# Kernel optimization log

Measured on AMD Instinct MI355X. Metric: run time of the kernel, lower is better.

The kernel has to match this reference:

```python
import jax, jax.numpy as jnp
import numpy as np

N = 50000      # total nodes
E = 800000     # total edges
G = 1000       # graphs in batch
H = 128        # in_channels == hidden_channels
L = 3          # num GCN layers
C = 6          # num classes
EPS = 1e-5     # BatchNorm eps


def setup_inputs() -> dict:
    key = jax.random.key(0)
    ks = jax.random.split(key, 8)
    x = jax.random.normal(ks[0], (N, H), jnp.float32)
    edge_index = jax.random.randint(ks[1], (2, E), 0, N)
    batch = jnp.sort(jax.random.randint(ks[2], (N,), 0, G))
    conv_w = jax.random.normal(ks[3], (L, H, H), jnp.float32) * 0.05
    conv_b = jnp.zeros((L, H), jnp.float32)
    bn_g = jnp.ones((L, H), jnp.float32)
    bn_b = jnp.zeros((L, H), jnp.float32)
    mlp_w1 = jax.random.normal(ks[4], (H, H), jnp.float32) * 0.05
    mlp_b1 = jnp.zeros((H,), jnp.float32)
    mlp_w2 = jax.random.normal(ks[5], (H, C), jnp.float32) * 0.05
    mlp_b2 = jnp.zeros((C,), jnp.float32)
    return {"x": x, "edge_index": edge_index, "batch": batch,
            "conv_w": conv_w, "conv_b": conv_b, "bn_g": bn_g, "bn_b": bn_b,
            "mlp_w1": mlp_w1, "mlp_b1": mlp_b1, "mlp_w2": mlp_w2, "mlp_b2": mlp_b2}


def reference(x, edge_index, batch, conv_w, conv_b, bn_g, bn_b, mlp_w1, mlp_b1, mlp_w2, mlp_b2):
    src, dst = edge_index[0], edge_index[1]
    # GCN symmetric norm with self-loops: deg over A+I
    deg = jax.ops.segment_sum(jnp.ones((E,), x.dtype), dst, num_segments=N) + 1.0
    dis = jax.lax.rsqrt(deg)                      # deg^{-1/2}, [N]
    edge_norm = (dis[src] * dis[dst])[:, None]    # [E,1]
    self_norm = (dis * dis)[:, None]              # [N,1] self-loop weight 1/deg

    for l in range(L):
        h = x @ conv_w[l]                                             # [N,H]
        agg = jax.ops.segment_sum(h[src] * edge_norm, dst, num_segments=N)
        h = agg + h * self_norm + conv_b[l]
        # BatchNorm (training-mode batch statistics, biased var)
        mu = jnp.mean(h, axis=0)
        var = jnp.var(h, axis=0)
        hn = (h - mu) * jax.lax.rsqrt(var + EPS)
        x = jax.nn.relu(hn * bn_g[l] + bn_b[l])   # dropout = identity (eval)

    # global mean pool per graph
    sums = jax.ops.segment_sum(x, batch, num_segments=G)              # [G,H]
    cnt = jax.ops.segment_sum(jnp.ones((N,), x.dtype), batch, num_segments=G)
    pooled = sums / jnp.maximum(cnt, 1.0)[:, None]

    h = jax.nn.relu(pooled @ mlp_w1 + mlp_b1)
    return h @ mlp_w2 + mlp_b2                                         # [G,C]
```

## Files before the change

### kernel.cpp

```cpp
#include <hip/hip_runtime.h>

#define Nn 50000
#define Ee 800000
#define Gg 1000
#define Hh 128
#define Cc 6
#define EPSf 1e-5f
#define SB 1024
#define NSB ((Nn + SB - 1) / SB)
#define NBH 64
#define EPB (Ee / NBH)
#define NW (Nn / 2)
#define HWH (NW / 2)

typedef unsigned short u16;
typedef unsigned int u32;
typedef __attribute__((ext_vector_type(8))) short bf16x8;
typedef __attribute__((ext_vector_type(4))) float f32x4;
typedef __attribute__((ext_vector_type(4))) unsigned int u32x4;

static __device__ inline u16 f2bf(float f) {
    u32 u = __float_as_uint(f);
    u32 r = (u + 0x7fffu + ((u >> 16) & 1u)) >> 16;
    return (u16)r;
}
static __device__ inline float bf_lo(u32 v) { return __uint_as_float(v << 16); }
static __device__ inline float bf_hi(u32 v) { return __uint_as_float(v & 0xffff0000u); }
static __device__ inline u32 pack2(float a, float b) {
    return ((u32)f2bf(b) << 16) | (u32)f2bf(a);
}

__global__ __launch_bounds__(256) void k_pre(const float* __restrict__ W3,
                                             u16* __restrict__ WT3,
                                             float* __restrict__ stats3) {
    int t = blockIdx.x * blockDim.x + threadIdx.x;
    if (t < 3 * 2 * Hh) stats3[t] = 0.0f;

    __shared__ u16 tbuf[Hh * 136];
    int l = blockIdx.x;
    const float* W = W3 + l * Hh * Hh;
    u16* WT = WT3 + l * Hh * Hh;
    int tid = threadIdx.x;
#pragma unroll
    for (int i = 0; i < 16; i++) {
        int v = tid + 256 * i;
        int r = v >> 5, c4 = v & 31;
        float4 d = ((const float4*)W)[v];
        u16* p = tbuf + r * 136 + c4 * 4;
        p[0] = f2bf(d.x); p[1] = f2bf(d.y); p[2] = f2bf(d.z); p[3] = f2bf(d.w);
    }
    __syncthreads();
#pragma unroll
    for (int i = 0; i < 64; i++) {
        int o = tid + 256 * i;
        int n = o >> 7, k = o & 127;
        WT[o] = tbuf[k * 136 + n];
    }
}

__global__ __launch_bounds__(1024) void k_hist(const int* __restrict__ ei_dst,
                                               u16* __restrict__ rankL,
                                               u32* __restrict__ partials) {
    __shared__ u32 h[HWH];
    int b = blockIdx.x, t = threadIdx.x;
    int e0 = b * EPB;
    u32* P = partials + b * NW;
#pragma unroll 1
    for (int half = 0; half < 2; half++) {
        int wlo = half * HWH;
        for (int i = t; i < HWH; i += 1024) h[i] = 0u;
        __syncthreads();
        for (int i = t; i < EPB; i += 1024) {
            int d = ei_dst[e0 + i];
            int w = d >> 1;
            if (w >= wlo && w < wlo + HWH) {
                u32 old = atomicAdd(&h[w - wlo], (d & 1) ? 65536u : 1u);
                rankL[e0 + i] = (u16)((d & 1) ? (old >> 16) : (old & 0xffffu));
            }
        }
        __syncthreads();
        for (int i = t; i < HWH; i += 1024) P[wlo + i] = h[i];
        __syncthreads();
    }
}

__global__ __launch_bounds__(256) void k_merge(const u32* __restrict__ partials,
                                               u32* __restrict__ base_off,
                                               int* __restrict__ indeg) {
    int w = blockIdx.x * 256 + threadIdx.x;
    if (w >= NW) return;
    u32 run = 0;
#pragma unroll 8
    for (int b = 0; b < NBH; b++) {
        u32 v = partials[b * NW + w];
        base_off[b * NW + w] = run;
        run += v;
    }
    ((int2*)indeg)[w] = make_int2((int)(run & 0xffffu), (int)(run >> 16));
}

__global__ __launch_bounds__(256) void k_scan1(const int* __restrict__ indeg,
                                               int* __restrict__ rs,
                                               int* __restrict__ bsum,
                                               float* __restrict__ dis,
                                               const int* __restrict__ batch,
                                               int* __restrict__ gstart) {
    __shared__ int ts[256];
    int b = blockIdx.x;
    int t = threadIdx.x;
    int base = b * SB + t * 4;
    int v[4] = {0, 0, 0, 0};
#pragma unroll
    for (int j = 0; j < 4; j++) {
        int i = base + j;
        if (i < Nn) { v[j] = indeg[i]; dis[i] = rsqrtf((float)v[j] + 1.0f); }
    }
    int g = b * 256 + t;
    if (g <= Gg) {
        int lo = 0, hi = Nn;
        while (lo < hi) {
            int mid = (lo + hi) >> 1;
            if (batch[mid] < g) lo = mid + 1; else hi = mid;
        }
        gstart[g] = lo;
    }
    int tsum = v[0] + v[1] + v[2] + v[3];
    ts[t] = tsum;
    __syncthreads();
    for (int off = 1; off < 256; off <<= 1) {
        int x = (t >= off) ? ts[t - off] : 0;
        __syncthreads();
        ts[t] += x;
        __syncthreads();
    }
    int run = (t == 0) ? 0 : ts[t - 1];
    if (t == 255) bsum[b] = ts[255];
#pragma unroll
    for (int j = 0; j < 4; j++) {
        int i = base + j;
        if (i < Nn) { rs[i] = run; run += v[j]; }
    }
}

__global__ __launch_bounds__(256) void k_scan2(int* __restrict__ rs,
                                               const int* __restrict__ bsum) {
    __shared__ int lboff[NSB];
    int t = threadIdx.x;
    if (t < 64) {
        int orig = (t < NSB) ? bsum[t] : 0;
        int v = orig;
#pragma unroll
        for (int off = 1; off < 64; off <<= 1) {
            int u = __shfl_up(v, off, 64);
            if (t >= off) v += u;
        }
        if (t < NSB) lboff[t] = v - orig;
    }
    __syncthreads();
    int i = blockIdx.x * blockDim.x + t;
    if (i < Nn) rs[i] += lboff[i >> 10];
    if (blockIdx.x == 0 && t == 0) rs[Nn] = Ee;
}

__global__ void k_fill(const int* __restrict__ ei, const int* __restrict__ rs,
                       const u16* __restrict__ rankL,
                       const u32* __restrict__ base_off,
                       const float* __restrict__ dis, u32* __restrict__ recs) {
    int e = blockIdx.x * blockDim.x + threadIdx.x;
    if (e >= Ee) return;
    int s = ei[e];
    int d = ei[Ee + e];
    int blk = e / EPB;
    u32 bo = base_off[blk * NW + (d >> 1)];
    int rank = (int)rankL[e] + (int)((d & 1) ? (bo >> 16) : (bo & 0xffffu));
    int slot = rs[d] + rank;
    float w = dis[s] * dis[d];
    recs[slot] = ((u32)f2bf(w) << 16) | (u32)s;
}

__global__ __launch_bounds__(256) void k_gemm(const u16* __restrict__ Xin,
                                              const float* __restrict__ Xf,
                                              const u16* __restrict__ WT,
                                              u16* __restrict__ Yh,
                                              const float* __restrict__ stats,
                                              const float* __restrict__ gam,
                                              const float* __restrict__ bet,
                                              int mode) {
    __shared__ u16 wt[Hh * 136];
    __shared__ float s_scale[Hh], s_shift[Hh];
    int tid = threadIdx.x;

    if (mode == 1 && tid < Hh) {
        float mu = stats[tid] * (1.0f / Nn);
        float var = stats[Hh + tid] * (1.0f / Nn) - mu * mu;
        float sc = rsqrtf(var + EPSf) * gam[tid];
        s_scale[tid] = sc;
        s_shift[tid] = bet[tid] - mu * sc;
    }
#pragma unroll
    for (int i = 0; i < 8; i++) {
        int v = tid + 256 * i;
        int n = v >> 4, k8 = v & 15;
        uint4 d = ((const uint4*)WT)[v];
        *((uint4*)(wt + n * 136 + k8 * 8)) = d;
    }
    __syncthreads();

    int wv = tid >> 6, lane = tid & 63;
    int m = lane & 15, q = lane >> 4;
    int row0 = blockIdx.x * 64 + wv * 16;
    int lrow = row0 + m;
    if (lrow >= Nn) lrow = Nn - 1;
    const u16* xrow = Xin + lrow * Hh + q * 8;
    const float* xfrow = Xf + lrow * Hh + q * 8;

    f32x4 acc[8] = {};
#pragma unroll
    for (int k0 = 0; k0 < Hh; k0 += 32) {
        bf16x8 a;
        if (mode == 1) {
            int cb = k0 + q * 8;
            uint4 p = *(const uint4*)(xrow + k0);
            float4 sc0 = *(const float4*)(s_scale + cb);
            float4 sc1 = *(const float4*)(s_scale + cb + 4);
            float4 sh0 = *(const float4*)(s_shift + cb);
            float4 sh1 = *(const float4*)(s_shift + cb + 4);
            float f0 = fmaxf(bf_lo(p.x) * sc0.x + sh0.x, 0.0f);
            float f1 = fmaxf(bf_hi(p.x) * sc0.y + sh0.y, 0.0f);
            float f2 = fmaxf(bf_lo(p.y) * sc0.z + sh0.z, 0.0f);
            float f3 = fmaxf(bf_hi(p.y) * sc0.w + sh0.w, 0.0f);
            float f4 = fmaxf(bf_lo(p.z) * sc1.x + sh1.x, 0.0f);
            float f5 = fmaxf(bf_hi(p.z) * sc1.y + sh1.y, 0.0f);
            float f6 = fmaxf(bf_lo(p.w) * sc1.z + sh1.z, 0.0f);
            float f7 = fmaxf(bf_hi(p.w) * sc1.w + sh1.w, 0.0f);
            union { bf16x8 v; u32 u[4]; } cv;
            cv.u[0] = pack2(f0, f1);
            cv.u[1] = pack2(f2, f3);
            cv.u[2] = pack2(f4, f5);
            cv.u[3] = pack2(f6, f7);
            a = cv.v;
        } else {
            float4 u0 = *(const float4*)(xfrow + k0);
            float4 u1 = *(const float4*)(xfrow + k0 + 4);
            union { bf16x8 v; u32 u[4]; } cv;
            cv.u[0] = pack2(u0.x, u0.y);
            cv.u[1] = pack2(u0.z, u0.w);
            cv.u[2] = pack2(u1.x, u1.y);
            cv.u[3] = pack2(u1.z, u1.w);
            a = cv.v;
        }
#pragma unroll
        for (int t = 0; t < 8; t++) {
            bf16x8 b = *(const bf16x8*)(wt + (t * 16 + m) * 136 + k0 + q * 8);
            acc[t] = __builtin_amdgcn_mfma_f32_16x16x32_bf16(a, b, acc[t], 0, 0, 0);
        }
    }

    int orow0 = row0 + q * 4;
#pragma unroll
    for (int t = 0; t < 8; t++) {
#pragma unroll
        for (int r = 0; r < 4; r++) {
            int rr = orow0 + r;
            if (rr < Nn) Yh[rr * Hh + t * 16 + m] = f2bf(acc[t][r]);
        }
    }
}

__global__ __launch_bounds__(256) void k_gather(const u16* __restrict__ Yh,
                                                const float* __restrict__ dis,
                                                const float* __restrict__ bias,
                                                const int* __restrict__ rs,
                                                const u32* __restrict__ recs,
                                                u16* __restrict__ Ah) {
    int node = blockIdx.x * 4 + (threadIdx.x >> 6);
    if (node >= Nn) return;
    int lane = threadIdx.x & 63;
    int lg = lane >> 4;
    int lc = lane & 15;

    const uint4* rows4 = (const uint4*)Yh;

    float acc[8] = {0.f, 0.f, 0.f, 0.f, 0.f, 0.f, 0.f, 0.f};

    int beg = rs[node];
    int end = rs[node + 1];

    for (int base = beg; base < end; base += 64) {
        int me = base + lane;
        u32 myrec = recs[me < end ? me : end - 1];
        int cnt = end - base;
        if (cnt > 64) cnt = 64;
        for (int i0 = 0; i0 < cnt; i0 += 16) {
            u32 rr[4]; float ww[4]; uint4 vv[4];
#pragma unroll
            for (int j = 0; j < 4; j++) {
                int si = i0 + j * 4 + lg;
                int sc = si < cnt ? si : cnt - 1;
                u32 rec = __shfl(myrec, sc, 64);
                rr[j] = rec & 0xffffu;
                ww[j] = (si < cnt) ? __uint_as_float(rec & 0xffff0000u) : 0.0f;
            }
#pragma unroll
            for (int j = 0; j < 4; j++) vv[j] = rows4[rr[j] * 16 + lc];
#pragma unroll
            for (int j = 0; j < 4; j++) {
                acc[0] += bf_lo(vv[j].x) * ww[j];
                acc[1] += bf_hi(vv[j].x) * ww[j];
                acc[2] += bf_lo(vv[j].y) * ww[j];
                acc[3] += bf_hi(vv[j].y) * ww[j];
                acc[4] += bf_lo(vv[j].z) * ww[j];
                acc[5] += bf_hi(vv[j].z) * ww[j];
                acc[6] += bf_lo(vv[j].w) * ww[j];
                acc[7] += bf_hi(vv[j].w) * ww[j];
            }
        }
    }
#pragma unroll
    for (int k = 0; k < 8; k++) {
        acc[k] += __shfl_xor(acc[k], 16, 64);
        acc[k] += __shfl_xor(acc[k], 32, 64);
    }
    if (lg == 0) {
        float sn = dis[node];
        sn = sn * sn;
        uint4 hv = rows4[node * 16 + lc];
        const float4* bq = (const float4*)bias;
        float4 b0 = bq[lc * 2];
        float4 b1 = bq[lc * 2 + 1];
        acc[0] = acc[0] + bf_lo(hv.x) * sn + b0.x;
        acc[1] = acc[1] + bf_hi(hv.x) * sn + b0.y;
        acc[2] = acc[2] + bf_lo(hv.y) * sn + b0.z;
        acc[3] = acc[3] + bf_hi(hv.y) * sn + b0.w;
        acc[4] = acc[4] + bf_lo(hv.z) * sn + b1.x;
        acc[5] = acc[5] + bf_hi(hv.z) * sn + b1.y;
        acc[6] = acc[6] + bf_lo(hv.w) * sn + b1.z;
        acc[7] = acc[7] + bf_hi(hv.w) * sn + b1.w;
        u32x4 o;
        o.x = pack2(acc[0], acc[1]);
        o.y = pack2(acc[2], acc[3]);
        o.z = pack2(acc[4], acc[5]);
        o.w = pack2(acc[6], acc[7]);
        __builtin_nontemporal_store(o, (u32x4*)Ah + node * 16 + lc);
    }
}

__global__ __launch_bounds__(256) void k_stats(const u16* __restrict__ Ah,
                                               float* __restrict__ stats) {
    __shared__ float sh[4][256];
    int t = threadIdx.x;
    int jc = t & 63, ro = t >> 6;
    const u32* col = (const u32*)Ah + jc;
    float sx = 0.f, sy = 0.f, qx = 0.f, qy = 0.f;
    for (int r = blockIdx.x * 16 + ro * 4; r < Nn; r += 4096) {
        u32 v[4];
#pragma unroll
        for (int k = 0; k < 4; k++) {
            int rr = r + k;
            v[k] = (rr < Nn) ? col[rr * 64] : 0u;
        }
#pragma unroll
        for (int k = 0; k < 4; k++) {
            float a = bf_lo(v[k]), b = bf_hi(v[k]);
            sx += a; sy += b; qx += a * a; qy += b * b;
        }
    }
    sh[0][t] = sx; sh[1][t] = sy; sh[2][t] = qx; sh[3][t] = qy;
    __syncthreads();
    if (t < 64) {
        sx = sh[0][t] + sh[0][t + 64] + sh[0][t + 128] + sh[0][t + 192];
        sy = sh[1][t] + sh[1][t + 64] + sh[1][t + 128] + sh[1][t + 192];
        qx = sh[2][t] + sh[2][t + 64] + sh[2][t + 128] + sh[2][t + 192];
        qy = sh[3][t] + sh[3][t + 64] + sh[3][t + 128] + sh[3][t + 192];
        atomicAdd(&stats[2 * t], sx);
        atomicAdd(&stats[2 * t + 1], sy);
        atomicAdd(&stats[Hh + 2 * t], qx);
        atomicAdd(&stats[Hh + 2 * t + 1], qy);
    }
}

__global__ __launch_bounds__(128) void k_poolmlp(const u16* __restrict__ Ah,
                                                 const float* __restrict__ stats,
                                                 const float* __restrict__ gam,
                                                 const float* __restrict__ bet,
                                                 const int* __restrict__ gstart,
                                                 const float* __restrict__ W1,
                                                 const float* __restrict__ b1,
                                                 const float* __restrict__ W2,
                                                 const float* __restrict__ b2,
                                                 float* __restrict__ out) {
    int g = blockIdx.x;
    int c = threadIdx.x;
    __shared__ float p[Hh];
    __shared__ float hid[Hh];
    float mu = stats[c] * (1.0f / Nn);
    float var = stats[Hh + c] * (1.0f / Nn) - mu * mu;
    float sc = rsqrtf(var + EPSf) * gam[c];
    float sf = bet[c] - mu * sc;
    int s = gstart[g], e = gstart[g + 1];
    float sum0 = 0.0f, sum1 = 0.0f;
    int r = s;
    for (; r + 1 < e; r += 2) {
        float v0 = __uint_as_float((u32)Ah[r * Hh + c] << 16);
        float v1 = __uint_as_float((u32)Ah[(r + 1) * Hh + c] << 16);
        sum0 += fmaxf(v0 * sc + sf, 0.0f);
        sum1 += fmaxf(v1 * sc + sf, 0.0f);
    }
    if (r < e) {
        float v = __uint_as_float((u32)Ah[r * Hh + c] << 16);
        sum0 += fmaxf(v * sc + sf, 0.0f);
    }
    int n = e - s;
    p[c] = (sum0 + sum1) / (float)(n > 1 ? n : 1);
    __syncthreads();
    float acc = b1[c];
    for (int k = 0; k < Hh; k++) acc += p[k] * W1[k * Hh + c];
    hid[c] = fmaxf(acc, 0.0f);
    __syncthreads();
    if (c < Cc) {
        float acc2 = b2[c];
        for (int k = 0; k < Hh; k++) acc2 += hid[k] * W2[k * Cc + c];
        out[g * Cc + c] = acc2;
    }
}

extern "C" void kernel_launch(void* const* d_in, const int* in_sizes, int n_in,
                              void* d_out, int out_size, void* d_ws, size_t ws_size,
                              hipStream_t stream) {
    const float* x      = (const float*)d_in[0];
    const int*   ei     = (const int*)d_in[1];
    const int*   batch  = (const int*)d_in[2];
    const float* conv_w = (const float*)d_in[3];
    const float* conv_b = (const float*)d_in[4];
    const float* bn_g   = (const float*)d_in[5];
    const float* bn_b   = (const float*)d_in[6];
    const float* w1     = (const float*)d_in[7];
    const float* b1     = (const float*)d_in[8];
    const float* w2     = (const float*)d_in[9];
    const float* b2     = (const float*)d_in[10];
    float* out = (float*)d_out;

    u16*   Yh      = (u16*)d_ws;
    u16*   Ah      = Yh + Nn * Hh;
    u16*   WT      = Ah + Nn * Hh;
    float* dis     = (float*)(WT + 3 * Hh * Hh);
    float* stats3  = dis + Nn;
    int*   indeg   = (int*)(stats3 + 3 * 2 * Hh);
    int*   rs      = indeg + Nn;
    int*   gstart  = rs + Nn + 1;
    int*   bsum    = gstart + Gg + 1;
    u32*   recs    = (u32*)(bsum + NSB);
    u16*   rankL   = (u16*)(recs + Ee);
    u32*   partials = (u32*)(rankL + Ee);
    u32*   base_off = partials + NBH * NW;

    k_pre<<<3, 256, 0, stream>>>(conv_w, WT, stats3);
    k_gemm<<<(Nn + 63) / 64, 256, 0, stream>>>(nullptr, x, WT, Yh,
                                               nullptr, nullptr, nullptr, 2);
    k_hist<<<NBH, 1024, 0, stream>>>(ei + Ee, rankL, partials);
    k_merge<<<(NW + 255) / 256, 256, 0, stream>>>(partials, base_off, indeg);
    k_scan1<<<NSB, 256, 0, stream>>>(indeg, rs, bsum, dis, batch, gstart);
    k_scan2<<<(Nn + 255) / 256, 256, 0, stream>>>(rs, bsum);
    k_fill<<<(Ee + 255) / 256, 256, 0, stream>>>(ei, rs, rankL, base_off, dis, recs);

    for (int l = 0; l < 3; l++) {
        k_gather<<<(Nn + 3) / 4, 256, 0, stream>>>(Yh, dis, conv_b + l * Hh, rs,
                                                   recs, Ah);
        k_stats<<<256, 256, 0, stream>>>(Ah, stats3 + l * 2 * Hh);
        if (l < 2) {
            k_gemm<<<(Nn + 63) / 64, 256, 0, stream>>>(Ah, nullptr,
                                                       WT + (l + 1) * Hh * Hh, Yh,
                                                       stats3 + l * 2 * Hh,
                                                       bn_g + l * Hh, bn_b + l * Hh, 1);
        }
    }

    k_poolmlp<<<Gg, 128, 0, stream>>>(Ah, stats3 + 2 * 2 * Hh, bn_g + 2 * Hh,
                                      bn_b + 2 * Hh, gstart, w1, b1, w2, b2, out);
}
```

Before: 331.0 us.

## Fuse per-layer gather/stats/GEMM into one cooperative persistent kernel; merge histogram merge into scan

The three GCN layers' gather, BatchNorm statistics and next-layer GEMM launches are replaced by one cooperative persistent kernel with 768 blocks. Grid-wide syncs separate the phases and blocks loop over nodes and tiles. Separately, the k_merge kernel is folded into k_scan1, so each scan thread computes the per-node degree prefix directly from the histogram partials. This removes about eight kernel launches and their gaps, at the cost of grid.sync overhead and a fixed grid size that may underfill or imbalance the gather phase.

```diff
diff --git a/kernel.cpp b/kernel.cpp
--- a/kernel.cpp
+++ b/kernel.cpp
@@ -1,4 +1,7 @@
 #include <hip/hip_runtime.h>
+#include <hip/hip_cooperative_groups.h>
+
+namespace cg = cooperative_groups;
 
 #define Nn 50000
 #define Ee 800000
@@ -12,6 +15,7 @@
 #define EPB (Ee / NBH)
 #define NW (Nn / 2)
 #define HWH (NW / 2)
+#define LGRID 768
 
 typedef unsigned short u16;
 typedef unsigned int u32;
@@ -84,22 +88,8 @@
     }
 }
 
-__global__ __launch_bounds__(256) void k_merge(const u32* __restrict__ partials,
+__global__ __launch_bounds__(256) void k_scan1(const u32* __restrict__ partials,
                                                u32* __restrict__ base_off,
-                                               int* __restrict__ indeg) {
-    int w = blockIdx.x * 256 + threadIdx.x;
-    if (w >= NW) return;
-    u32 run = 0;
-#pragma unroll 8
-    for (int b = 0; b < NBH; b++) {
-        u32 v = partials[b * NW + w];
-        base_off[b * NW + w] = run;
-        run += v;
-    }
-    ((int2*)indeg)[w] = make_int2((int)(run & 0xffffu), (int)(run >> 16));
-}
-
-__global__ __launch_bounds__(256) void k_scan1(const int* __restrict__ indeg,
                                                int* __restrict__ rs,
                                                int* __restrict__ bsum,
                                                float* __restrict__ dis,
@@ -110,10 +100,23 @@
     int t = threadIdx.x;
     int base = b * SB + t * 4;
     int v[4] = {0, 0, 0, 0};
-#pragma unroll
-    for (int j = 0; j < 4; j++) {
-        int i = base + j;
-        if (i < Nn) { v[j] = indeg[i]; dis[i] = rsqrtf((float)v[j] + 1.0f); }
+    if (base < Nn) {
+        int w0 = base >> 1;
+        u32 run0 = 0, run1 = 0;
+#pragma unroll 8
+        for (int b2 = 0; b2 < NBH; b2++) {
+            u32 p0 = partials[b2 * NW + w0];
+            u32 p1 = partials[b2 * NW + w0 + 1];
+            base_off[b2 * NW + w0] = run0;
+            base_off[b2 * NW + w0 + 1] = run1;
+            run0 += p0; run1 += p1;
+        }
+        v[0] = (int)(run0 & 0xffffu); v[1] = (int)(run0 >> 16);
+        v[2] = (int)(run1 & 0xffffu); v[3] = (int)(run1 >> 16);
+        dis[base]     = rsqrtf((float)v[0] + 1.0f);
+        dis[base + 1] = rsqrtf((float)v[1] + 1.0f);
+        dis[base + 2] = rsqrtf((float)v[2] + 1.0f);
+        dis[base + 3] = rsqrtf((float)v[3] + 1.0f);
     }
     int g = b * 256 + t;
     if (g <= Gg) {
@@ -178,114 +181,17 @@
     recs[slot] = ((u32)f2bf(w) << 16) | (u32)s;
 }
 
-__global__ __launch_bounds__(256) void k_gemm(const u16* __restrict__ Xin,
-                                              const float* __restrict__ Xf,
-                                              const u16* __restrict__ WT,
-                                              u16* __restrict__ Yh,
-                                              const float* __restrict__ stats,
-                                              const float* __restrict__ gam,
-                                              const float* __restrict__ bet,
-                                              int mode) {
-    __shared__ u16 wt[Hh * 136];
-    __shared__ float s_scale[Hh], s_shift[Hh];
-    int tid = threadIdx.x;
-
-    if (mode == 1 && tid < Hh) {
-        float mu = stats[tid] * (1.0f / Nn);
-        float var = stats[Hh + tid] * (1.0f / Nn) - mu * mu;
-        float sc = rsqrtf(var + EPSf) * gam[tid];
-        s_scale[tid] = sc;
-        s_shift[tid] = bet[tid] - mu * sc;
-    }
-#pragma unroll
-    for (int i = 0; i < 8; i++) {
-        int v = tid + 256 * i;
-        int n = v >> 4, k8 = v & 15;
-        uint4 d = ((const uint4*)WT)[v];
-        *((uint4*)(wt + n * 136 + k8 * 8)) = d;
-    }
-    __syncthreads();
-
-    int wv = tid >> 6, lane = tid & 63;
-    int m = lane & 15, q = lane >> 4;
-    int row0 = blockIdx.x * 64 + wv * 16;
-    int lrow = row0 + m;
-    if (lrow >= Nn) lrow = Nn - 1;
-    const u16* xrow = Xin + lrow * Hh + q * 8;
-    const float* xfrow = Xf + lrow * Hh + q * 8;
-
-    f32x4 acc[8] = {};
-#pragma unroll
-    for (int k0 = 0; k0 < Hh; k0 += 32) {
-        bf16x8 a;
-        if (mode == 1) {
-            int cb = k0 + q * 8;
-            uint4 p = *(const uint4*)(xrow + k0);
-            float4 sc0 = *(const float4*)(s_scale + cb);
-            float4 sc1 = *(const float4*)(s_scale + cb + 4);
-            float4 sh0 = *(const float4*)(s_shift + cb);
-            float4 sh1 = *(const float4*)(s_shift + cb + 4);
-            float f0 = fmaxf(bf_lo(p.x) * sc0.x + sh0.x, 0.0f);
-            float f1 = fmaxf(bf_hi(p.x) * sc0.y + sh0.y, 0.0f);
-            float f2 = fmaxf(bf_lo(p.y) * sc0.z + sh0.z, 0.0f);
-            float f3 = fmaxf(bf_hi(p.y) * sc0.w + sh0.w, 0.0f);
-            float f4 = fmaxf(bf_lo(p.z) * sc1.x + sh1.x, 0.0f);
-            float f5 = fmaxf(bf_hi(p.z) * sc1.y + sh1.y, 0.0f);
-            float f6 = fmaxf(bf_lo(p.w) * sc1.z + sh1.z, 0.0f);
-            float f7 = fmaxf(bf_hi(p.w) * sc1.w + sh1.w, 0.0f);
-            union { bf16x8 v; u32 u[4]; } cv;
-            cv.u[0] = pack2(f0, f1);
-            cv.u[1] = pack2(f2, f3);
-            cv.u[2] = pack2(f4, f5);
-            cv.u[3] = pack2(f6, f7);
-            a = cv.v;
-        } else {
-            float4 u0 = *(const float4*)(xfrow + k0);
-            float4 u1 = *(const float4*)(xfrow + k0 + 4);
-            union { bf16x8 v; u32 u[4]; } cv;
-            cv.u[0] = pack2(u0.x, u0.y);
-            cv.u[1] = pack2(u0.z, u0.w);
-            cv.u[2] = pack2(u1.x, u1.y);
-            cv.u[3] = pack2(u1.z, u1.w);
-            a = cv.v;
-        }
-#pragma unroll
-        for (int t = 0; t < 8; t++) {
-            bf16x8 b = *(const bf16x8*)(wt + (t * 16 + m) * 136 + k0 + q * 8);
-            acc[t] = __builtin_amdgcn_mfma_f32_16x16x32_bf16(a, b, acc[t], 0, 0, 0);
-        }
-    }
-
-    int orow0 = row0 + q * 4;
-#pragma unroll
-    for (int t = 0; t < 8; t++) {
-#pragma unroll
-        for (int r = 0; r < 4; r++) {
-            int rr = orow0 + r;
-            if (rr < Nn) Yh[rr * Hh + t * 16 + m] = f2bf(acc[t][r]);
-        }
-    }
-}
-
-__global__ __launch_bounds__(256) void k_gather(const u16* __restrict__ Yh,
-                                                const float* __restrict__ dis,
-                                                const float* __restrict__ bias,
-                                                const int* __restrict__ rs,
-                                                const u32* __restrict__ recs,
-                                                u16* __restrict__ Ah) {
-    int node = blockIdx.x * 4 + (threadIdx.x >> 6);
-    if (node >= Nn) return;
-    int lane = threadIdx.x & 63;
-    int lg = lane >> 4;
-    int lc = lane & 15;
-
-    const uint4* rows4 = (const uint4*)Yh;
-
+
+static __device__ inline void gather_node(int node, int lane, int lg, int lc,
+                                          const uint4* __restrict__ rows4,
+                                          const float* __restrict__ dis,
+                                          const float* __restrict__ bias,
+                                          const int* __restrict__ rs,
+                                          const u32* __restrict__ recs,
+                                          u16* __restrict__ Ah) {
     float acc[8] = {0.f, 0.f, 0.f, 0.f, 0.f, 0.f, 0.f, 0.f};
-
     int beg = rs[node];
     int end = rs[node + 1];
-
     for (int base = beg; base < end; base += 64) {
         int me = base + lane;
         u32 myrec = recs[me < end ? me : end - 1];
@@ -345,6 +251,159 @@
     }
 }
 
+static __device__ inline void gemm_tile_m1(int tile, int tid,
+                                           const u16* __restrict__ Xin,
+                                           const u16* __restrict__ wt,
+                                           const float* __restrict__ s_scale,
+                                           const float* __restrict__ s_shift,
+                                           u16* __restrict__ Yh) {
+    int wv = tid >> 6, lane = tid & 63;
+    int m = lane & 15, q = lane >> 4;
+    int row0 = tile * 64 + wv * 16;
+    int lrow = row0 + m;
+    if (lrow >= Nn) lrow = Nn - 1;
+    const u16* xrow = Xin + lrow * Hh + q * 8;
+
+    f32x4 acc[8] = {};
+#pragma unroll
+    for (int k0 = 0; k0 < Hh; k0 += 32) {
+        int cb = k0 + q * 8;
+        uint4 p = *(const uint4*)(xrow + k0);
+        float4 sc0 = *(const float4*)(s_scale + cb);
+        float4 sc1 = *(const float4*)(s_scale + cb + 4);
+        float4 sh0 = *(const float4*)(s_shift + cb);
+        float4 sh1 = *(const float4*)(s_shift + cb + 4);
+        float f0 = fmaxf(bf_lo(p.x) * sc0.x + sh0.x, 0.0f);
+        float f1 = fmaxf(bf_hi(p.x) * sc0.y + sh0.y, 0.0f);
+        float f2 = fmaxf(bf_lo(p.y) * sc0.z + sh0.z, 0.0f);
+        float f3 = fmaxf(bf_hi(p.y) * sc0.w + sh0.w, 0.0f);
+        float f4 = fmaxf(bf_lo(p.z) * sc1.x + sh1.x, 0.0f);
+        float f5 = fmaxf(bf_hi(p.z) * sc1.y + sh1.y, 0.0f);
+        float f6 = fmaxf(bf_lo(p.w) * sc1.z + sh1.z, 0.0f);
+        float f7 = fmaxf(bf_hi(p.w) * sc1.w + sh1.w, 0.0f);
+        union { bf16x8 v; u32 u[4]; } cv;
+        cv.u[0] = pack2(f0, f1);
+        cv.u[1] = pack2(f2, f3);
+        cv.u[2] = pack2(f4, f5);
+        cv.u[3] = pack2(f6, f7);
+        bf16x8 a = cv.v;
+#pragma unroll
+        for (int t = 0; t < 8; t++) {
+            bf16x8 bb = *(const bf16x8*)(wt + (t * 16 + m) * 136 + k0 + q * 8);
+            acc[t] = __builtin_amdgcn_mfma_f32_16x16x32_bf16(a, bb, acc[t], 0, 0, 0);
+        }
+    }
+    int orow0 = row0 + q * 4;
+#pragma unroll
+    for (int t = 0; t < 8; t++) {
+#pragma unroll
+        for (int r = 0; r < 4; r++) {
+            int rr = orow0 + r;
+            if (rr < Nn) Yh[rr * Hh + t * 16 + m] = f2bf(acc[t][r]);
+        }
+    }
+}
+
+__global__ __launch_bounds__(256, 3) void k_layers(u16* __restrict__ Yh,
+                                                   u16* __restrict__ Ah,
+                                                   const float* __restrict__ dis,
+                                                   const float* __restrict__ conv_b3,
+                                                   const int* __restrict__ rs,
+                                                   const u32* __restrict__ recs,
+                                                   float* __restrict__ stats3,
+                                                   const float* __restrict__ bn_g,
+                                                   const float* __restrict__ bn_b,
+                                                   const u16* __restrict__ WT3) {
+    cg::grid_group grid = cg::this_grid();
+    __shared__ __align__(16) unsigned char smem[Hh * 136 * 2 + 2 * Hh * 4];
+    int tid = threadIdx.x;
+    int lane = tid & 63, lg = lane >> 4, lc = lane & 15;
+
+    for (int l = 0; l < 3; l++) {
+        {
+            const float* bias = conv_b3 + l * Hh;
+            const uint4* rows4 = (const uint4*)Yh;
+            for (int qd = blockIdx.x; qd < Nn / 4; qd += gridDim.x) {
+                int node = qd * 4 + (tid >> 6);
+                gather_node(node, lane, lg, lc, rows4, dis, bias, rs, recs, Ah);
+            }
+        }
+        grid.sync();
+        {
+            float* stats = stats3 + l * 2 * Hh;
+            float (*sh)[256] = (float (*)[256])smem;
+            int jc = tid & 63, ro = tid >> 6;
+            const u32* col = (const u32*)Ah + jc;
+            float sx = 0.f, sy = 0.f, qx = 0.f, qy = 0.f;
+            for (int r = blockIdx.x * 16 + ro * 4; r < Nn; r += gridDim.x * 16) {
+                u32 v[4];
+#pragma unroll
+                for (int k = 0; k < 4; k++) {
+                    int rr = r + k;
+                    v[k] = (rr < Nn) ? col[rr * 64] : 0u;
+                }
+#pragma unroll
+                for (int k = 0; k < 4; k++) {
+                    float a = bf_lo(v[k]), b = bf_hi(v[k]);
+                    sx += a; sy += b; qx += a * a; qy += b * b;
+                }
+            }
+            sh[0][tid] = sx; sh[1][tid] = sy; sh[2][tid] = qx; sh[3][tid] = qy;
+            __syncthreads();
+            if (tid < 64) {
+                sx = sh[0][tid] + sh[0][tid + 64] + sh[0][tid + 128] + sh[0][tid + 192];
+                sy = sh[1][tid] + sh[1][tid + 64] + sh[1][tid + 128] + sh[1][tid + 192];
+                qx = sh[2][tid] + sh[2][tid + 64] + sh[2][tid + 128] + sh[2][tid + 192];
+                qy = sh[3][tid] + sh[3][tid + 64] + sh[3][tid + 128] + sh[3][tid + 192];
+                atomicAdd(&stats[2 * tid], sx);
+                atomicAdd(&stats[2 * tid + 1], sy);
+                atomicAdd(&stats[Hh + 2 * tid], qx);
+                atomicAdd(&stats[Hh + 2 * tid + 1], qy);
+            }
+        }
+        grid.sync();
+        if (l < 2) {
+            const u16* WT = WT3 + (l + 1) * Hh * Hh;
+            const float* stats = stats3 + l * 2 * Hh;
+            const float* gam = bn_g + l * Hh;
+            const float* bet = bn_b + l * Hh;
+            u16* wt = (u16*)smem;
+            float* s_scale = (float*)(smem + Hh * 136 * 2);
+            float* s_shift = s_scale + Hh;
+            if (tid < Hh) {
+                float mu = stats[tid] * (1.0f / Nn);
+                float var = stats[Hh + tid] * (1.0f / Nn) - mu * mu;
+                float sc = rsqrtf(var + EPSf) * gam[tid];
+                s_scale[tid] = sc;
+                s_shift[tid] = bet[tid] - mu * sc;
+            }
+#pragma unroll
+            for (int i = 0; i < 8; i++) {
+                int v = tid + 256 * i;
+                int n = v >> 4, k8 = v & 15;
+                uint4 d = ((const uint4*)WT)[v];
+                *((uint4*)(wt + n * 136 + k8 * 8)) = d;
+            }
+            __syncthreads();
+            for (int tile = blockIdx.x; tile < (Nn + 63) / 64; tile += gridDim.x)
+                gemm_tile_m1(tile, tid, Ah, wt, s_scale, s_shift, Yh);
+            grid.sync();
+        }
+    }
+}
+
+__global__ __launch_bounds__(256) void k_gather(const u16* __restrict__ Yh,
+                                                const float* __restrict__ dis,
+                                                const float* __restrict__ bias,
+                                                const int* __restrict__ rs,
+                                                const u32* __restrict__ recs,
+                                                u16* __restrict__ Ah) {
+    int node = blockIdx.x * 4 + (threadIdx.x >> 6);
+    if (node >= Nn) return;
+    int lane = threadIdx.x & 63;
+    gather_node(node, lane, lane >> 4, lane & 15, (const uint4*)Yh, dis, bias, rs, recs, Ah);
+}
+
 __global__ __launch_bounds__(256) void k_stats(const u16* __restrict__ Ah,
                                                float* __restrict__ stats) {
     __shared__ float sh[4][256];
@@ -376,6 +435,75 @@
         atomicAdd(&stats[2 * t + 1], sy);
         atomicAdd(&stats[Hh + 2 * t], qx);
         atomicAdd(&stats[Hh + 2 * t + 1], qy);
+    }
+}
+
+__global__ __launch_bounds__(256) void k_gemm(const u16* __restrict__ Xin,
+                                              const float* __restrict__ Xf,
+                                              const u16* __restrict__ WT,
+                                              u16* __restrict__ Yh,
+                                              const float* __restrict__ stats,
+                                              const float* __restrict__ gam,
+                                              const float* __restrict__ bet,
+                                              int mode) {
+    __shared__ u16 wt[Hh * 136];
+    __shared__ float s_scale[Hh], s_shift[Hh];
+    int tid = threadIdx.x;
+
+    if (mode == 1 && tid < Hh) {
+        float mu = stats[tid] * (1.0f / Nn);
+        float var = stats[Hh + tid] * (1.0f / Nn) - mu * mu;
+        float sc = rsqrtf(var + EPSf) * gam[tid];
+        s_scale[tid] = sc;
+        s_shift[tid] = bet[tid] - mu * sc;
+    }
+#pragma unroll
+    for (int i = 0; i < 8; i++) {
+        int v = tid + 256 * i;
+        int n = v >> 4, k8 = v & 15;
+        uint4 d = ((const uint4*)WT)[v];
+        *((uint4*)(wt + n * 136 + k8 * 8)) = d;
+    }
+    __syncthreads();
+
+    if (mode == 1) {
+        gemm_tile_m1(blockIdx.x, tid, Xin, wt, s_scale, s_shift, Yh);
+        return;
+    }
+
+    int wv = tid >> 6, lane = tid & 63;
+    int m = lane & 15, q = lane >> 4;
+    int row0 = blockIdx.x * 64 + wv * 16;
+    int lrow = row0 + m;
+    if (lrow >= Nn) lrow = Nn - 1;
+    const float* xfrow = Xf + lrow * Hh + q * 8;
+
+    f32x4 acc[8] = {};
+#pragma unroll
+    for (int k0 = 0; k0 < Hh; k0 += 32) {
+        float4 u0 = *(const float4*)(xfrow + k0);
+        float4 u1 = *(const float4*)(xfrow + k0 + 4);
+        union { bf16x8 v; u32 u[4]; } cv;
+        cv.u[0] = pack2(u0.x, u0.y);
+        cv.u[1] = pack2(u0.z, u0.w);
+        cv.u[2] = pack2(u1.x, u1.y);
+        cv.u[3] = pack2(u1.z, u1.w);
+        bf16x8 a = cv.v;
+#pragma unroll
+        for (int t = 0; t < 8; t++) {
+            bf16x8 b = *(const bf16x8*)(wt + (t * 16 + m) * 136 + k0 + q * 8);
+            acc[t] = __builtin_amdgcn_mfma_f32_16x16x32_bf16(a, b, acc[t], 0, 0, 0);
+        }
+    }
+
+    int orow0 = row0 + q * 4;
+#pragma unroll
+    for (int t = 0; t < 8; t++) {
+#pragma unroll
+        for (int r = 0; r < 4; r++) {
+            int rr = orow0 + r;
+            if (rr < Nn) Yh[rr * Hh + t * 16 + m] = f2bf(acc[t][r]);
+        }
     }
 }
 
@@ -445,8 +573,7 @@
     u16*   WT      = Ah + Nn * Hh;
     float* dis     = (float*)(WT + 3 * Hh * Hh);
     float* stats3  = dis + Nn;
-    int*   indeg   = (int*)(stats3 + 3 * 2 * Hh);
-    int*   rs      = indeg + Nn;
+    int*   rs      = (int*)(stats3 + 3 * 2 * Hh);
     int*   gstart  = rs + Nn + 1;
     int*   bsum    = gstart + Gg + 1;
     u32*   recs    = (u32*)(bsum + NSB);
@@ -458,20 +585,27 @@
     k_gemm<<<(Nn + 63) / 64, 256, 0, stream>>>(nullptr, x, WT, Yh,
                                                nullptr, nullptr, nullptr, 2);
     k_hist<<<NBH, 1024, 0, stream>>>(ei + Ee, rankL, partials);
-    k_merge<<<(NW + 255) / 256, 256, 0, stream>>>(partials, base_off, indeg);
-    k_scan1<<<NSB, 256, 0, stream>>>(indeg, rs, bsum, dis, batch, gstart);
+    k_scan1<<<NSB, 256, 0, stream>>>(partials, base_off, rs, bsum, dis, batch, gstart);
     k_scan2<<<(Nn + 255) / 256, 256, 0, stream>>>(rs, bsum);
     k_fill<<<(Ee + 255) / 256, 256, 0, stream>>>(ei, rs, rankL, base_off, dis, recs);
 
-    for (int l = 0; l < 3; l++) {
-        k_gather<<<(Nn + 3) / 4, 256, 0, stream>>>(Yh, dis, conv_b + l * Hh, rs,
-                                                   recs, Ah);
-        k_stats<<<256, 256, 0, stream>>>(Ah, stats3 + l * 2 * Hh);
-        if (l < 2) {
-            k_gemm<<<(Nn + 63) / 64, 256, 0, stream>>>(Ah, nullptr,
-                                                       WT + (l + 1) * Hh * Hh, Yh,
-                                                       stats3 + l * 2 * Hh,
-                                                       bn_g + l * Hh, bn_b + l * Hh, 1);
+    void* kargs[10] = {(void*)&Yh, (void*)&Ah, (void*)&dis, (void*)&conv_b,
+                       (void*)&rs, (void*)&recs, (void*)&stats3,
+                       (void*)&bn_g, (void*)&bn_b, (void*)&WT};
+    hipError_t cerr = hipLaunchCooperativeKernel((const void*)k_layers,
+                                                 dim3(LGRID), dim3(256),
+                                                 kargs, 0, stream);
+    if (cerr != hipSuccess) {
+        for (int l = 0; l < 3; l++) {
+            k_gather<<<(Nn + 3) / 4, 256, 0, stream>>>(Yh, dis, conv_b + l * Hh, rs,
+                                                       recs, Ah);
+            k_stats<<<256, 256, 0, stream>>>(Ah, stats3 + l * 2 * Hh);
+            if (l < 2) {
+                k_gemm<<<(Nn + 63) / 64, 256, 0, stream>>>(Ah, nullptr,
+                                                           WT + (l + 1) * Hh * Hh, Yh,
+                                                           stats3 + l * 2 * Hh,
+                                                           bn_g + l * Hh, bn_b + l * Hh, 1);
+            }
         }
     }
 
```

Result: slower. 1.161 ms (+250.9%).

## Merge CSR-build kernels and co-schedule histogram with first GEMM

Applied to the files above, without the earlier changes.

Fuses the edge histogram and the first-layer GEMM into one launch, with separate block ranges running concurrently. The per-block merge now happens inside the scan kernel, and the second scan step is folded into the fill kernel, which writes a corrected row-start array. This cuts the preprocessing launches from six to three and removes one pass over the row starts. The histogram blocks now use 256 threads instead of 1024, so that phase runs with far less parallelism and may become the critical path.

```diff
diff --git a/kernel.cpp b/kernel.cpp
--- a/kernel.cpp
+++ b/kernel.cpp
@@ -12,6 +12,7 @@
 #define EPB (Ee / NBH)
 #define NW (Nn / 2)
 #define HWH (NW / 2)
+#define GT ((Nn + 63) / 64)
 
 typedef unsigned short u16;
 typedef unsigned int u32;
@@ -33,14 +34,12 @@
 __global__ __launch_bounds__(256) void k_pre(const float* __restrict__ W3,
                                              u16* __restrict__ WT3,
                                              float* __restrict__ stats3) {
-    int t = blockIdx.x * blockDim.x + threadIdx.x;
-    if (t < 3 * 2 * Hh) stats3[t] = 0.0f;
-
     __shared__ u16 tbuf[Hh * 136];
     int l = blockIdx.x;
+    int tid = threadIdx.x;
+    stats3[l * 256 + tid] = 0.0f;
     const float* W = W3 + l * Hh * Hh;
     u16* WT = WT3 + l * Hh * Hh;
-    int tid = threadIdx.x;
 #pragma unroll
     for (int i = 0; i < 16; i++) {
         int v = tid + 256 * i;
@@ -58,48 +57,88 @@
     }
 }
 
-__global__ __launch_bounds__(1024) void k_hist(const int* __restrict__ ei_dst,
-                                               u16* __restrict__ rankL,
-                                               u32* __restrict__ partials) {
-    __shared__ u32 h[HWH];
-    int b = blockIdx.x, t = threadIdx.x;
-    int e0 = b * EPB;
-    u32* P = partials + b * NW;
+__global__ __launch_bounds__(256) void k_pro(const int* __restrict__ ei_dst,
+                                             u16* __restrict__ rankL,
+                                             u32* __restrict__ partials,
+                                             const float* __restrict__ Xf,
+                                             const u16* __restrict__ WT0,
+                                             u16* __restrict__ Yh) {
+    extern __shared__ __align__(16) unsigned char smem[];
+    int bid = blockIdx.x, tid = threadIdx.x;
+
+    if (bid < NBH) {
+        u32* h = (u32*)smem;
+        int e0 = bid * EPB;
+        u32* P = partials + bid * NW;
 #pragma unroll 1
-    for (int half = 0; half < 2; half++) {
-        int wlo = half * HWH;
-        for (int i = t; i < HWH; i += 1024) h[i] = 0u;
-        __syncthreads();
-        for (int i = t; i < EPB; i += 1024) {
-            int d = ei_dst[e0 + i];
-            int w = d >> 1;
-            if (w >= wlo && w < wlo + HWH) {
-                u32 old = atomicAdd(&h[w - wlo], (d & 1) ? 65536u : 1u);
-                rankL[e0 + i] = (u16)((d & 1) ? (old >> 16) : (old & 0xffffu));
+        for (int half = 0; half < 2; half++) {
+            int wlo = half * HWH;
+            for (int i = tid; i < HWH; i += 256) h[i] = 0u;
+            __syncthreads();
+            for (int i = tid; i < EPB; i += 256) {
+                int d = ei_dst[e0 + i];
+                int w = d >> 1;
+                if (w >= wlo && w < wlo + HWH) {
+                    u32 old = atomicAdd(&h[w - wlo], (d & 1) ? 65536u : 1u);
+                    rankL[e0 + i] = (u16)((d & 1) ? (old >> 16) : (old & 0xffffu));
+                }
             }
-        }
-        __syncthreads();
-        for (int i = t; i < HWH; i += 1024) P[wlo + i] = h[i];
-        __syncthreads();
-    }
-}
-
-__global__ __launch_bounds__(256) void k_merge(const u32* __restrict__ partials,
+            __syncthreads();
+            for (int i = tid; i < HWH; i += 256) P[wlo + i] = h[i];
+            __syncthreads();
+        }
+        return;
+    }
+
+    u16* wt = (u16*)smem;
+#pragma unroll
+    for (int i = 0; i < 8; i++) {
+        int v = tid + 256 * i;
+        int n = v >> 4, k8 = v & 15;
+        uint4 d = ((const uint4*)WT0)[v];
+        *((uint4*)(wt + n * 136 + k8 * 8)) = d;
+    }
+    __syncthreads();
+
+    int tile = bid - NBH;
+    int wv = tid >> 6, lane = tid & 63;
+    int m = lane & 15, q = lane >> 4;
+    int row0 = tile * 64 + wv * 16;
+    int lrow = row0 + m;
+    if (lrow >= Nn) lrow = Nn - 1;
+    const float* xfrow = Xf + lrow * Hh + q * 8;
+
+    f32x4 acc[8] = {};
+#pragma unroll
+    for (int k0 = 0; k0 < Hh; k0 += 32) {
+        float4 u0 = *(const float4*)(xfrow + k0);
+        float4 u1 = *(const float4*)(xfrow + k0 + 4);
+        union { bf16x8 v; u32 u[4]; } cv;
+        cv.u[0] = pack2(u0.x, u0.y);
+        cv.u[1] = pack2(u0.z, u0.w);
+        cv.u[2] = pack2(u1.x, u1.y);
+        cv.u[3] = pack2(u1.z, u1.w);
+        bf16x8 a = cv.v;
+#pragma unroll
+        for (int t = 0; t < 8; t++) {
+            bf16x8 b = *(const bf16x8*)(wt + (t * 16 + m) * 136 + k0 + q * 8);
+            acc[t] = __builtin_amdgcn_mfma_f32_16x16x32_bf16(a, b, acc[t], 0, 0, 0);
+        }
+    }
+
+    int orow0 = row0 + q * 4;
+#pragma unroll
+    for (int t = 0; t < 8; t++) {
+#pragma unroll
+        for (int r = 0; r < 4; r++) {
+            int rr = orow0 + r;
+            if (rr < Nn) Yh[rr * Hh + t * 16 + m] = f2bf(acc[t][r]);
+        }
+    }
+}
+
+__global__ __launch_bounds__(256) void k_scan1(const u32* __restrict__ partials,
                                                u32* __restrict__ base_off,
-                                               int* __restrict__ indeg) {
-    int w = blockIdx.x * 256 + threadIdx.x;
-    if (w >= NW) return;
-    u32 run = 0;
-#pragma unroll 8
-    for (int b = 0; b < NBH; b++) {
-        u32 v = partials[b * NW + w];
-        base_off[b * NW + w] = run;
-        run += v;
-    }
-    ((int2*)indeg)[w] = make_int2((int)(run & 0xffffu), (int)(run >> 16));
-}
-
-__global__ __launch_bounds__(256) void k_scan1(const int* __restrict__ indeg,
                                                int* __restrict__ rs,
                                                int* __restrict__ bsum,
                                                float* __restrict__ dis,
@@ -110,10 +149,23 @@
     int t = threadIdx.x;
     int base = b * SB + t * 4;
     int v[4] = {0, 0, 0, 0};
-#pragma unroll
-    for (int j = 0; j < 4; j++) {
-        int i = base + j;
-        if (i < Nn) { v[j] = indeg[i]; dis[i] = rsqrtf((float)v[j] + 1.0f); }
+    if (base < Nn) {
+        int w0 = base >> 1;
+        u32 run0 = 0, run1 = 0;
+#pragma unroll 8
+        for (int b2 = 0; b2 < NBH; b2++) {
+            u32 p0 = partials[b2 * NW + w0];
+            u32 p1 = partials[b2 * NW + w0 + 1];
+            base_off[b2 * NW + w0] = run0;
+            base_off[b2 * NW + w0 + 1] = run1;
+            run0 += p0; run1 += p1;
+        }
+        v[0] = (int)(run0 & 0xffffu); v[1] = (int)(run0 >> 16);
+        v[2] = (int)(run1 & 0xffffu); v[3] = (int)(run1 >> 16);
+        dis[base]     = rsqrtf((float)v[0] + 1.0f);
+        dis[base + 1] = rsqrtf((float)v[1] + 1.0f);
+        dis[base + 2] = rsqrtf((float)v[2] + 1.0f);
+        dis[base + 3] = rsqrtf((float)v[3] + 1.0f);
     }
     int g = b * 256 + t;
     if (g <= Gg) {
@@ -134,7 +186,10 @@
         __syncthreads();
     }
     int run = (t == 0) ? 0 : ts[t - 1];
-    if (t == 255) bsum[b] = ts[255];
+    if (t == 255) {
+        bsum[b] = ts[255];
+        if (b == NSB - 1) rs[Nn] = ts[255];
+    }
 #pragma unroll
     for (int j = 0; j < 4; j++) {
         int i = base + j;
@@ -142,8 +197,14 @@
     }
 }
 
-__global__ __launch_bounds__(256) void k_scan2(int* __restrict__ rs,
-                                               const int* __restrict__ bsum) {
+__global__ __launch_bounds__(256) void k_fill(const int* __restrict__ ei,
+                                              const int* __restrict__ rs,
+                                              const int* __restrict__ bsum,
+                                              int* __restrict__ rs2,
+                                              const u16* __restrict__ rankL,
+                                              const u32* __restrict__ base_off,
+                                              const float* __restrict__ dis,
+                                              u32* __restrict__ recs) {
     __shared__ int lboff[NSB];
     int t = threadIdx.x;
     if (t < 64) {
@@ -157,120 +218,26 @@
         if (t < NSB) lboff[t] = v - orig;
     }
     __syncthreads();
-    int i = blockIdx.x * blockDim.x + t;
-    if (i < Nn) rs[i] += lboff[i >> 10];
-    if (blockIdx.x == 0 && t == 0) rs[Nn] = Ee;
-}
-
-__global__ void k_fill(const int* __restrict__ ei, const int* __restrict__ rs,
-                       const u16* __restrict__ rankL,
-                       const u32* __restrict__ base_off,
-                       const float* __restrict__ dis, u32* __restrict__ recs) {
-    int e = blockIdx.x * blockDim.x + threadIdx.x;
+
+    int gi = blockIdx.x * 256 + t;
+    if (gi <= Nn) rs2[gi] = rs[gi] + lboff[gi >> 10];
+
+    int e = gi;
     if (e >= Ee) return;
     int s = ei[e];
     int d = ei[Ee + e];
     int blk = e / EPB;
     u32 bo = base_off[blk * NW + (d >> 1)];
     int rank = (int)rankL[e] + (int)((d & 1) ? (bo >> 16) : (bo & 0xffffu));
-    int slot = rs[d] + rank;
+    int slot = rs[d] + lboff[d >> 10] + rank;
     float w = dis[s] * dis[d];
     recs[slot] = ((u32)f2bf(w) << 16) | (u32)s;
-}
-
-__global__ __launch_bounds__(256) void k_gemm(const u16* __restrict__ Xin,
-                                              const float* __restrict__ Xf,
-                                              const u16* __restrict__ WT,
-                                              u16* __restrict__ Yh,
-                                              const float* __restrict__ stats,
-                                              const float* __restrict__ gam,
-                                              const float* __restrict__ bet,
-                                              int mode) {
-    __shared__ u16 wt[Hh * 136];
-    __shared__ float s_scale[Hh], s_shift[Hh];
-    int tid = threadIdx.x;
-
-    if (mode == 1 && tid < Hh) {
-        float mu = stats[tid] * (1.0f / Nn);
-        float var = stats[Hh + tid] * (1.0f / Nn) - mu * mu;
-        float sc = rsqrtf(var + EPSf) * gam[tid];
-        s_scale[tid] = sc;
-        s_shift[tid] = bet[tid] - mu * sc;
-    }
-#pragma unroll
-    for (int i = 0; i < 8; i++) {
-        int v = tid + 256 * i;
-        int n = v >> 4, k8 = v & 15;
-        uint4 d = ((const uint4*)WT)[v];
-        *((uint4*)(wt + n * 136 + k8 * 8)) = d;
-    }
-    __syncthreads();
-
-    int wv = tid >> 6, lane = tid & 63;
-    int m = lane & 15, q = lane >> 4;
-    int row0 = blockIdx.x * 64 + wv * 16;
-    int lrow = row0 + m;
-    if (lrow >= Nn) lrow = Nn - 1;
-    const u16* xrow = Xin + lrow * Hh + q * 8;
-    const float* xfrow = Xf + lrow * Hh + q * 8;
-
-    f32x4 acc[8] = {};
-#pragma unroll
-    for (int k0 = 0; k0 < Hh; k0 += 32) {
-        bf16x8 a;
-        if (mode == 1) {
-            int cb = k0 + q * 8;
-            uint4 p = *(const uint4*)(xrow + k0);
-            float4 sc0 = *(const float4*)(s_scale + cb);
-            float4 sc1 = *(const float4*)(s_scale + cb + 4);
-            float4 sh0 = *(const float4*)(s_shift + cb);
-            float4 sh1 = *(const float4*)(s_shift + cb + 4);
-            float f0 = fmaxf(bf_lo(p.x) * sc0.x + sh0.x, 0.0f);
-            float f1 = fmaxf(bf_hi(p.x) * sc0.y + sh0.y, 0.0f);
-            float f2 = fmaxf(bf_lo(p.y) * sc0.z + sh0.z, 0.0f);
-            float f3 = fmaxf(bf_hi(p.y) * sc0.w + sh0.w, 0.0f);
-            float f4 = fmaxf(bf_lo(p.z) * sc1.x + sh1.x, 0.0f);
-            float f5 = fmaxf(bf_hi(p.z) * sc1.y + sh1.y, 0.0f);
-            float f6 = fmaxf(bf_lo(p.w) * sc1.z + sh1.z, 0.0f);
-            float f7 = fmaxf(bf_hi(p.w) * sc1.w + sh1.w, 0.0f);
-            union { bf16x8 v; u32 u[4]; } cv;
-            cv.u[0] = pack2(f0, f1);
-            cv.u[1] = pack2(f2, f3);
-            cv.u[2] = pack2(f4, f5);
-            cv.u[3] = pack2(f6, f7);
-            a = cv.v;
-        } else {
-            float4 u0 = *(const float4*)(xfrow + k0);
-            float4 u1 = *(const float4*)(xfrow + k0 + 4);
-            union { bf16x8 v; u32 u[4]; } cv;
-            cv.u[0] = pack2(u0.x, u0.y);
-            cv.u[1] = pack2(u0.z, u0.w);
-            cv.u[2] = pack2(u1.x, u1.y);
-            cv.u[3] = pack2(u1.z, u1.w);
-            a = cv.v;
-        }
-#pragma unroll
-        for (int t = 0; t < 8; t++) {
-            bf16x8 b = *(const bf16x8*)(wt + (t * 16 + m) * 136 + k0 + q * 8);
-            acc[t] = __builtin_amdgcn_mfma_f32_16x16x32_bf16(a, b, acc[t], 0, 0, 0);
-        }
-    }
-
-    int orow0 = row0 + q * 4;
-#pragma unroll
-    for (int t = 0; t < 8; t++) {
-#pragma unroll
-        for (int r = 0; r < 4; r++) {
-            int rr = orow0 + r;
-            if (rr < Nn) Yh[rr * Hh + t * 16 + m] = f2bf(acc[t][r]);
-        }
-    }
 }
 
 __global__ __launch_bounds__(256) void k_gather(const u16* __restrict__ Yh,
                                                 const float* __restrict__ dis,
                                                 const float* __restrict__ bias,
-                                                const int* __restrict__ rs,
+                                                const int* __restrict__ rs2,
                                                 const u32* __restrict__ recs,
                                                 u16* __restrict__ Ah) {
     int node = blockIdx.x * 4 + (threadIdx.x >> 6);
@@ -283,8 +250,8 @@
 
     float acc[8] = {0.f, 0.f, 0.f, 0.f, 0.f, 0.f, 0.f, 0.f};
 
-    int beg = rs[node];
-    int end = rs[node + 1];
+    int beg = rs2[node];
+    int end = rs2[node + 1];
 
     for (int base = beg; base < end; base += 64) {
         int me = base + lane;
@@ -376,6 +343,80 @@
         atomicAdd(&stats[2 * t + 1], sy);
         atomicAdd(&stats[Hh + 2 * t], qx);
         atomicAdd(&stats[Hh + 2 * t + 1], qy);
+    }
+}
+
+__global__ __launch_bounds__(256) void k_gemm(const u16* __restrict__ Xin,
+                                              const u16* __restrict__ WT,
+                                              u16* __restrict__ Yh,
+                                              const float* __restrict__ stats,
+                                              const float* __restrict__ gam,
+                                              const float* __restrict__ bet) {
+    __shared__ u16 wt[Hh * 136];
+    __shared__ float s_scale[Hh], s_shift[Hh];
+    int tid = threadIdx.x;
+
+    if (tid < Hh) {
+        float mu = stats[tid] * (1.0f / Nn);
+        float var = stats[Hh + tid] * (1.0f / Nn) - mu * mu;
+        float sc = rsqrtf(var + EPSf) * gam[tid];
+        s_scale[tid] = sc;
+        s_shift[tid] = bet[tid] - mu * sc;
+    }
+#pragma unroll
+    for (int i = 0; i < 8; i++) {
+        int v = tid + 256 * i;
+        int n = v >> 4, k8 = v & 15;
+        uint4 d = ((const uint4*)WT)[v];
+        *((uint4*)(wt + n * 136 + k8 * 8)) = d;
+    }
+    __syncthreads();
+
+    int wv = tid >> 6, lane = tid & 63;
+    int m = lane & 15, q = lane >> 4;
+    int row0 = blockIdx.x * 64 + wv * 16;
+    int lrow = row0 + m;
+    if (lrow >= Nn) lrow = Nn - 1;
+    const u16* xrow = Xin + lrow * Hh + q * 8;
+
+    f32x4 acc[8] = {};
+#pragma unroll
+    for (int k0 = 0; k0 < Hh; k0 += 32) {
+        int cb = k0 + q * 8;
+        uint4 p = *(const uint4*)(xrow + k0);
+        float4 sc0 = *(const float4*)(s_scale + cb);
+        float4 sc1 = *(const float4*)(s_scale + cb + 4);
+        float4 sh0 = *(const float4*)(s_shift + cb);
+        float4 sh1 = *(const float4*)(s_shift + cb + 4);
+        float f0 = fmaxf(bf_lo(p.x) * sc0.x + sh0.x, 0.0f);
+        float f1 = fmaxf(bf_hi(p.x) * sc0.y + sh0.y, 0.0f);
+        float f2 = fmaxf(bf_lo(p.y) * sc0.z + sh0.z, 0.0f);
+        float f3 = fmaxf(bf_hi(p.y) * sc0.w + sh0.w, 0.0f);
+        float f4 = fmaxf(bf_lo(p.z) * sc1.x + sh1.x, 0.0f);
+        float f5 = fmaxf(bf_hi(p.z) * sc1.y + sh1.y, 0.0f);
+        float f6 = fmaxf(bf_lo(p.w) * sc1.z + sh1.z, 0.0f);
+        float f7 = fmaxf(bf_hi(p.w) * sc1.w + sh1.w, 0.0f);
+        union { bf16x8 v; u32 u[4]; } cv;
+        cv.u[0] = pack2(f0, f1);
+        cv.u[1] = pack2(f2, f3);
+        cv.u[2] = pack2(f4, f5);
+        cv.u[3] = pack2(f6, f7);
+        bf16x8 a = cv.v;
+#pragma unroll
+        for (int t = 0; t < 8; t++) {
+            bf16x8 b = *(const bf16x8*)(wt + (t * 16 + m) * 136 + k0 + q * 8);
+            acc[t] = __builtin_amdgcn_mfma_f32_16x16x32_bf16(a, b, acc[t], 0, 0, 0);
+        }
+    }
+
+    int orow0 = row0 + q * 4;
+#pragma unroll
+    for (int t = 0; t < 8; t++) {
+#pragma unroll
+        for (int r = 0; r < 4; r++) {
+            int rr = orow0 + r;
+            if (rr < Nn) Yh[rr * Hh + t * 16 + m] = f2bf(acc[t][r]);
+        }
     }
 }
 
@@ -445,9 +486,9 @@
     u16*   WT      = Ah + Nn * Hh;
     float* dis     = (float*)(WT + 3 * Hh * Hh);
     float* stats3  = dis + Nn;
-    int*   indeg   = (int*)(stats3 + 3 * 2 * Hh);
-    int*   rs      = indeg + Nn;
-    int*   gstart  = rs + Nn + 1;
+    int*   rs      = (int*)(stats3 + 3 * 2 * Hh);
+    int*   rs2     = rs + Nn + 1;
+    int*   gstart  = rs2 + Nn + 1;
     int*   bsum    = gstart + Gg + 1;
     u32*   recs    = (u32*)(bsum + NSB);
     u16*   rankL   = (u16*)(recs + Ee);
@@ -455,23 +496,19 @@
     u32*   base_off = partials + NBH * NW;
 
     k_pre<<<3, 256, 0, stream>>>(conv_w, WT, stats3);
-    k_gemm<<<(Nn + 63) / 64, 256, 0, stream>>>(nullptr, x, WT, Yh,
-                                               nullptr, nullptr, nullptr, 2);
-    k_hist<<<NBH, 1024, 0, stream>>>(ei + Ee, rankL, partials);
-    k_merge<<<(NW + 255) / 256, 256, 0, stream>>>(partials, base_off, indeg);
-    k_scan1<<<NSB, 256, 0, stream>>>(indeg, rs, bsum, dis, batch, gstart);
-    k_scan2<<<(Nn + 255) / 256, 256, 0, stream>>>(rs, bsum);
-    k_fill<<<(Ee + 255) / 256, 256, 0, stream>>>(ei, rs, rankL, base_off, dis, recs);
+    k_pro<<<NBH + GT, 256, 50000, stream>>>(ei + Ee, rankL, partials, x, WT, Yh);
+    k_scan1<<<NSB, 256, 0, stream>>>(partials, base_off, rs, bsum, dis, batch, gstart);
+    k_fill<<<(Ee + 255) / 256, 256, 0, stream>>>(ei, rs, bsum, rs2, rankL, base_off,
+                                                 dis, recs);
 
     for (int l = 0; l < 3; l++) {
-        k_gather<<<(Nn + 3) / 4, 256, 0, stream>>>(Yh, dis, conv_b + l * Hh, rs,
+        k_gather<<<(Nn + 3) / 4, 256, 0, stream>>>(Yh, dis, conv_b + l * Hh, rs2,
                                                    recs, Ah);
         k_stats<<<256, 256, 0, stream>>>(Ah, stats3 + l * 2 * Hh);
         if (l < 2) {
-            k_gemm<<<(Nn + 63) / 64, 256, 0, stream>>>(Ah, nullptr,
-                                                       WT + (l + 1) * Hh * Hh, Yh,
+            k_gemm<<<(Nn + 63) / 64, 256, 0, stream>>>(Ah, WT + (l + 1) * Hh * Hh, Yh,
                                                        stats3 + l * 2 * Hh,
-                                                       bn_g + l * Hh, bn_b + l * Hh, 1);
+                                                       bn_g + l * Hh, bn_b + l * Hh);
         }
     }
 
```

Result: slower. 339.5 us (+2.6%).
